# Kernel optimization log

Hardware: AMD Instinct MI355X
Metric: run time of the kernel (lower is better)

The kernel has to match this reference:

```python
import jax, jax.numpy as jnp
import numpy as np

D = 1024
H = 16
DH = D // H


def setup_inputs() -> dict:
    key = jax.random.key(0)
    ks = jax.random.split(key, 5)
    x = jax.random.normal(ks[0], (2, 2048, D), dtype=jnp.float32)
    s = 1.0 / np.sqrt(D)
    W_qkv = jax.random.normal(ks[1], (D, 3 * D), dtype=jnp.float32) * s
    b_qkv = jnp.zeros((3 * D,), dtype=jnp.float32)
    W_out = jax.random.normal(ks[2], (D, D), dtype=jnp.float32) * s
    b_out = jnp.zeros((D,), dtype=jnp.float32)
    return {"x": x, "W_qkv": W_qkv, "b_qkv": b_qkv, "W_out": W_out, "b_out": b_out}


def reference(x, W_qkv, b_qkv, W_out, b_out):
    B, N, _ = x.shape
    qkv = x @ W_qkv + b_qkv                       # [B,N,3D]
    qkv = qkv.reshape(B, N, 3, H, DH)
    q = jnp.transpose(qkv[:, :, 0], (0, 2, 1, 3))  # [B,H,N,DH]
    k = jnp.transpose(qkv[:, :, 1], (0, 2, 1, 3))
    v = jnp.transpose(qkv[:, :, 2], (0, 2, 1, 3))
    scores = jnp.einsum('bhnd,bhmd->bhnm', q, k) / jnp.sqrt(jnp.float32(DH))
    attn = jax.nn.softmax(scores, axis=-1)
    out = jnp.einsum('bhnm,bhmd->bhnd', attn, v)   # [B,H,N,DH]
    out = jnp.transpose(out, (0, 2, 1, 3)).reshape(B, N, D)
    return out @ W_out + b_out
```

## Files before the change

kernel.cpp:

```cpp
#include <hip/hip_runtime.h>

typedef unsigned short u16;
typedef unsigned int u32;
typedef __attribute__((ext_vector_type(8))) short bf16x8;
typedef __attribute__((ext_vector_type(4))) float f32x4;

static __device__ __forceinline__ void mfma16(f32x4& c, bf16x8 a, bf16x8 b) {
  asm("v_mfma_f32_16x16x32_bf16 %0, %1, %2, %0" : "+v"(c) : "v"(a), "v"(b));
}
static __device__ __forceinline__ float exp2_fast(float x) {
  float r; asm("v_exp_f32 %0, %1" : "=v"(r) : "v"(x)); return r;
}
static __device__ __forceinline__ u32 cvt_pk_bf16(float lo, float hi) {
  u32 r; asm("v_cvt_pk_bf16_f32 %0, %1, %2" : "=v"(r) : "v"(lo), "v"(hi)); return r;
}

static __device__ __forceinline__ float bfly_sum(float x) {
  x += __shfl_xor(x, 16);
  x += __shfl_xor(x, 32);
  return x;
}

static __device__ __forceinline__ u16 f2bf(float f) {
  union { float f; u32 u; } v; v.f = f;
  u32 r = v.u + 0x7fffu + ((v.u >> 16) & 1u);
  return (u16)(r >> 16);
}

typedef __attribute__((address_space(1))) void as1_v;
typedef __attribute__((address_space(3))) void as3_v;
static __device__ __forceinline__ void gload16(const u16* g, u16* l) {
  __builtin_amdgcn_global_load_lds((as1_v*)g, (as3_v*)l, 16, 0, 0);
}

__global__ __launch_bounds__(256) void cvt_bf16(const float* __restrict__ in,
                                                u16* __restrict__ out, int n4) {
  int i = blockIdx.x * 256 + threadIdx.x;
  if (i < n4) {
    float4 f = ((const float4*)in)[i];
    ushort4 u;
    u.x = f2bf(f.x); u.y = f2bf(f.y); u.z = f2bf(f.z); u.w = f2bf(f.w);
    ((ushort4*)out)[i] = u;
  }
}

__global__ __launch_bounds__(256) void transpose_cvt(const float* __restrict__ W,
                                                     u16* __restrict__ Wt,
                                                     int K, int Nc) {
  __shared__ float tile[32][33];
  int nb = blockIdx.x * 32, kb = blockIdx.y * 32;
  int tx = threadIdx.x, ty = threadIdx.y;
  for (int i = ty; i < 32; i += 8)
    tile[i][tx] = W[(size_t)(kb + i) * Nc + nb + tx];
  __syncthreads();
  for (int i = ty; i < 32; i += 8)
    Wt[(size_t)(nb + i) * K + kb + tx] = f2bf(tile[tx][i]);
}

__global__ __launch_bounds__(256) void vtrans(const u16* __restrict__ qkv,
                                              u16* __restrict__ vt) {
  __shared__ u16 t[64][72];
  const int tid = threadIdx.x;
  const int bh = blockIdx.y, nt = blockIdx.x;
  const int b = bh >> 4, h = bh & 15;
  const int n0 = nt * 64;
  const int r = tid >> 3, c = tid & 7;
  const u16* src = qkv + (size_t)(b * 2048 + n0 + r) * 3072 + 2048 + h * 64;
  *(int4*)&t[r][(c ^ ((r >> 3) & 7)) * 8] = *(const int4*)(src + c * 8);
  const u16* src2 = src + (size_t)32 * 3072;
  *(int4*)&t[r + 32][(c ^ (((r + 32) >> 3) & 7)) * 8] = *(const int4*)(src2 + c * 8);
  __syncthreads();
  const int d = tid >> 3, j0 = (tid & 7) * 8;
  union { int4 v; u16 u[8]; } o0, o1;
#pragma unroll
  for (int j = 0; j < 8; ++j) {
    const int row = j0 + j;
    const int sw = (row >> 3) & 7;
    o0.u[j] = t[row][((d >> 3) ^ sw) * 8 + (d & 7)];
    o1.u[j] = t[row][(((d + 32) >> 3) ^ sw) * 8 + ((d + 32) & 7)];
  }
  u16* dst = vt + (size_t)bh * 131072 + (size_t)d * 2048 + n0 + j0;
  *(int4*)dst = o0.v;
  *(int4*)(dst + (size_t)32 * 2048) = o1.v;
}

template <int OUT_F32>
__global__ __launch_bounds__(256) void gemm_bt(const u16* __restrict__ A,
                                               const u16* __restrict__ Bt,
                                               const float* __restrict__ bias,
                                               void* __restrict__ C,
                                               int M, int N, int K,
                                               float qscale, int qcols) {
  __shared__ u16 lA[2][4096];
  __shared__ u16 lB[2][4096];
  const int tid = threadIdx.x;
  const int lane = tid & 63, wid = tid >> 6;
  const int nbx = N >> 7;
  const int per = ((M >> 7) * nbx) >> 3;
  const int g = (blockIdx.x & 7) * per + (blockIdx.x >> 3);
  const int bx = g % nbx, by = g / nbx;
  const int m0 = by << 7, n0 = bx << 7;
  const int wr = wid >> 1, wc = wid & 1;

  const int srow = tid >> 2;
  const int scol = (tid & 3) << 3;
  const u16* gA0 = A + (size_t)(m0 + srow) * K + scol;
  const u16* gA1 = A + (size_t)(m0 + 64 + srow) * K + scol;
  const u16* gB0 = Bt + (size_t)(n0 + srow) * K + scol;
  const u16* gB1 = Bt + (size_t)(n0 + 64 + srow) * K + scol;

  const int rdA = (wr * 64 + (lane & 15)) * 32 + ((lane >> 4) * 8);
  const int rdB = (wc * 64 + (lane & 15)) * 32 + ((lane >> 4) * 8);

  f32x4 acc[4][4] = {};

  gload16(gA0, &lA[0][tid * 8]);
  gload16(gA1, &lA[0][2048 + tid * 8]);
  gload16(gB0, &lB[0][tid * 8]);
  gload16(gB1, &lB[0][2048 + tid * 8]);
  __syncthreads();

  const int nk = K >> 5;
  for (int t = 0; t < nk; ++t) {
    const int cur = t & 1, nxt = cur ^ 1;
    if (t + 1 < nk) {
      const int k0 = (t + 1) << 5;
      gload16(gA0 + k0, &lA[nxt][tid * 8]);
      gload16(gA1 + k0, &lA[nxt][2048 + tid * 8]);
      gload16(gB0 + k0, &lB[nxt][tid * 8]);
      gload16(gB1 + k0, &lB[nxt][2048 + tid * 8]);
    }
    bf16x8 aF[4], bF[4];
#pragma unroll
    for (int m = 0; m < 4; ++m) aF[m] = *(const bf16x8*)(&lA[cur][rdA + m * 512]);
#pragma unroll
    for (int n = 0; n < 4; ++n) bF[n] = *(const bf16x8*)(&lB[cur][rdB + n * 512]);
#pragma unroll
    for (int m = 0; m < 4; ++m)
#pragma unroll
      for (int n = 0; n < 4; ++n) mfma16(acc[m][n], aF[m], bF[n]);
    __syncthreads();
  }

#pragma unroll
  for (int n = 0; n < 4; ++n) {
    const int col = n0 + wc * 64 + n * 16 + (lane & 15);
    const float bv = bias[col];
    const float sc = (col < qcols) ? qscale : 1.0f;
#pragma unroll
    for (int m = 0; m < 4; ++m) {
      const int rbase = m0 + wr * 64 + m * 16 + ((lane >> 4) * 4);
#pragma unroll
      for (int r = 0; r < 4; ++r) {
        const float v = (acc[m][n][r] + bv) * sc;
        const size_t idx = (size_t)(rbase + r) * N + col;
        if (OUT_F32) ((float*)C)[idx] = v;
        else         ((u16*)C)[idx] = f2bf(v);
      }
    }
  }
}

__global__ __launch_bounds__(256) void gemm_bt_n64(const u16* __restrict__ A,
                                                   const u16* __restrict__ Bt,
                                                   const float* __restrict__ bias,
                                                   float* __restrict__ C,
                                                   int M, int N, int K) {
  __shared__ u16 lA[2][4096];
  __shared__ u16 lB[2][2048];
  const int tid = threadIdx.x;
  const int lane = tid & 63, wid = tid >> 6;
  const int nbx = N >> 6;
  const int per = ((M >> 7) * nbx) >> 3;
  const int g = (blockIdx.x & 7) * per + (blockIdx.x >> 3);
  const int bx = g % nbx, by = g / nbx;
  const int m0 = by << 7, n0 = bx << 6;
  const int wr = wid >> 1, wc = wid & 1;

  const int srow = tid >> 2;
  const int scol = (tid & 3) << 3;
  const u16* gA0 = A + (size_t)(m0 + srow) * K + scol;
  const u16* gA1 = A + (size_t)(m0 + 64 + srow) * K + scol;
  const u16* gB0 = Bt + (size_t)(n0 + srow) * K + scol;

  const int rdA = (wr * 64 + (lane & 15)) * 32 + ((lane >> 4) * 8);
  const int rdB = (wc * 32 + (lane & 15)) * 32 + ((lane >> 4) * 8);

  f32x4 acc[4][2] = {};

  gload16(gA0, &lA[0][tid * 8]);
  gload16(gA1, &lA[0][2048 + tid * 8]);
  gload16(gB0, &lB[0][tid * 8]);
  __syncthreads();

  const int nk = K >> 5;
  for (int t = 0; t < nk; ++t) {
    const int cur = t & 1, nxt = cur ^ 1;
    if (t + 1 < nk) {
      const int k0 = (t + 1) << 5;
      gload16(gA0 + k0, &lA[nxt][tid * 8]);
      gload16(gA1 + k0, &lA[nxt][2048 + tid * 8]);
      gload16(gB0 + k0, &lB[nxt][tid * 8]);
    }
    bf16x8 aF[4], bF[2];
#pragma unroll
    for (int m = 0; m < 4; ++m) aF[m] = *(const bf16x8*)(&lA[cur][rdA + m * 512]);
#pragma unroll
    for (int n = 0; n < 2; ++n) bF[n] = *(const bf16x8*)(&lB[cur][rdB + n * 512]);
#pragma unroll
    for (int m = 0; m < 4; ++m)
#pragma unroll
      for (int n = 0; n < 2; ++n) mfma16(acc[m][n], aF[m], bF[n]);
    __syncthreads();
  }

#pragma unroll
  for (int n = 0; n < 2; ++n) {
    const int col = n0 + wc * 32 + n * 16 + (lane & 15);
    const float bv = bias[col];
#pragma unroll
    for (int m = 0; m < 4; ++m) {
      const int rbase = m0 + wr * 64 + m * 16 + ((lane >> 4) * 4);
#pragma unroll
      for (int r = 0; r < 4; ++r)
        C[(size_t)(rbase + r) * N + col] = acc[m][n][r] + bv;
    }
  }
}

__global__ __launch_bounds__(256) void attn_kernel(const u16* __restrict__ qkv,
                                                   const u16* __restrict__ vt,
                                                   u16* __restrict__ attn_out) {
  __shared__ u16 lK[2][4096];
  __shared__ u16 lV[2][4096];

  const int tid = threadIdx.x, lane = tid & 63, w = tid >> 6;
  const int l15 = lane & 15, g = lane >> 4;
  const int bid = blockIdx.x;
  const int tt = bid >> 3;
  const int qt = tt & 31;
  const int bh = ((tt >> 5) << 3) | (bid & 7);
  const int b = bh >> 4, h = bh & 15;

  const size_t rowQ = (size_t)(b * 2048 + qt * 64 + w * 16 + l15);
  const u16* qptr = qkv + rowQ * 3072 + h * 64 + g * 8;
  const bf16x8 qf0 = *(const bf16x8*)(qptr);
  const bf16x8 qf1 = *(const bf16x8*)(qptr + 32);

  const int r0 = tid >> 3, r1 = 32 + (tid >> 3);
  const int c0 = (tid & 7) ^ ((r0 ^ (r0 >> 3)) & 7);
  const int c1 = (tid & 7) ^ ((r1 ^ (r1 >> 3)) & 7);
  const u16* gk0 = qkv + (size_t)(b * 2048 + r0) * 3072 + 1024 + h * 64 + c0 * 8;
  const u16* gk1 = qkv + (size_t)(b * 2048 + r1) * 3072 + 1024 + h * 64 + c1 * 8;
  const u16* vtb = vt + (size_t)bh * 131072;
  const u16* gv0 = vtb + (size_t)r0 * 2048 + c0 * 8;
  const u16* gv1 = vtb + (size_t)r1 * 2048 + c1 * 8;

  int koff[4][2];
#pragma unroll
  for (int f = 0; f < 4; ++f) {
    const int R = 32 * (f >> 1) + 8 * (l15 >> 2) + 4 * ((l15 >> 1) & 1) +
                  2 * (f & 1) + (l15 & 1);
    const int sw = (R ^ (R >> 3)) & 7;
#pragma unroll
    for (int hf = 0; hf < 2; ++hf)
      koff[f][hf] = R * 64 + ((((hf << 2) | g) ^ sw) << 3);
  }
  int voff[4][2];
#pragma unroll
  for (int d = 0; d < 4; ++d) {
    const int R = d * 16 + l15;
    const int sw = (R ^ (R >> 3)) & 7;
#pragma unroll
    for (int kk = 0; kk < 2; ++kk)
      voff[d][kk] = R * 64 + ((((kk << 2) | g) ^ sw) << 3);
  }

  float lp = 0.f;
  f32x4 oacc[4] = {};

  gload16(gk0, &lK[0][tid * 8]);
  gload16(gk1, &lK[0][2048 + tid * 8]);
  gload16(gv0, &lV[0][tid * 8]);
  gload16(gv1, &lV[0][2048 + tid * 8]);
  __syncthreads();

  for (int it = 0; it < 32; ++it) {
    const int cur = it & 1, nxt = cur ^ 1;
    const u16* Kc = lK[cur];
    const u16* Vc = lV[cur];
    if (it + 1 < 32) {
      const size_t ko = (size_t)(it + 1) * 64 * 3072;
      const int vo = (it + 1) * 64;
      gload16(gk0 + ko, &lK[nxt][tid * 8]);
      gload16(gk1 + ko, &lK[nxt][2048 + tid * 8]);
      gload16(gv0 + vo, &lV[nxt][tid * 8]);
      gload16(gv1 + vo, &lV[nxt][2048 + tid * 8]);
    }

    f32x4 s[4] = {};
#pragma unroll
    for (int f = 0; f < 4; ++f) {
      mfma16(s[f], *(const bf16x8*)(Kc + koff[f][0]), qf0);
      mfma16(s[f], *(const bf16x8*)(Kc + koff[f][1]), qf1);
    }

#pragma unroll
    for (int f = 0; f < 4; ++f)
#pragma unroll
      for (int r = 0; r < 4; ++r) s[f][r] = exp2_fast(s[f][r]);
    lp += (((s[0][0] + s[0][1]) + (s[0][2] + s[0][3])) +
           ((s[1][0] + s[1][1]) + (s[1][2] + s[1][3]))) +
          (((s[2][0] + s[2][1]) + (s[2][2] + s[2][3])) +
           ((s[3][0] + s[3][1]) + (s[3][2] + s[3][3])));

    union { bf16x8 v; u32 u[4]; } p0, p1;
    p0.u[0] = cvt_pk_bf16(s[0][0], s[0][1]);
    p0.u[1] = cvt_pk_bf16(s[1][0], s[1][1]);
    p0.u[2] = cvt_pk_bf16(s[0][2], s[0][3]);
    p0.u[3] = cvt_pk_bf16(s[1][2], s[1][3]);
    p1.u[0] = cvt_pk_bf16(s[2][0], s[2][1]);
    p1.u[1] = cvt_pk_bf16(s[3][0], s[3][1]);
    p1.u[2] = cvt_pk_bf16(s[2][2], s[2][3]);
    p1.u[3] = cvt_pk_bf16(s[3][2], s[3][3]);

#pragma unroll
    for (int d = 0; d < 4; ++d) {
      mfma16(oacc[d], *(const bf16x8*)(Vc + voff[d][0]), p0.v);
      mfma16(oacc[d], *(const bf16x8*)(Vc + voff[d][1]), p1.v);
    }

    __syncthreads();
  }

  const float l_ = bfly_sum(lp);
  const float inv = 1.f / l_;
#pragma unroll
  for (int d = 0; d < 4; ++d)
#pragma unroll
    for (int r = 0; r < 4; ++r)
      attn_out[rowQ * 1024 + h * 64 + d * 16 + g * 4 + r] = f2bf(oacc[d][r] * inv);
}

extern "C" void kernel_launch(void* const* d_in, const int* in_sizes, int n_in,
                              void* d_out, int out_size, void* d_ws, size_t ws_size,
                              hipStream_t stream) {
  const float* x    = (const float*)d_in[0];
  const float* Wqkv = (const float*)d_in[1];
  const float* bqkv = (const float*)d_in[2];
  const float* Wout = (const float*)d_in[3];
  const float* bout = (const float*)d_in[4];
  float* out = (float*)d_out;

  char* ws = (char*)d_ws;
  u16* xb    = (u16*)(ws);
  u16* vt    = (u16*)(ws);
  u16* WqkvT = (u16*)(ws + 8388608);
  u16* WoutT = (u16*)(ws + 14680064);
  u16* qkvb  = (u16*)(ws + 16777216);
  u16* attnb = (u16*)(ws + 41943040);

  cvt_bf16<<<4096, 256, 0, stream>>>(x, xb, 4194304 / 4);
  transpose_cvt<<<dim3(96, 32), dim3(32, 8), 0, stream>>>(Wqkv, WqkvT, 1024, 3072);
  transpose_cvt<<<dim3(32, 32), dim3(32, 8), 0, stream>>>(Wout, WoutT, 1024, 1024);

  gemm_bt<0><<<dim3(24 * 32), 256, 0, stream>>>(xb, WqkvT, bqkv, qkvb,
                                                4096, 3072, 1024, 0.18033688f, 1024);
  vtrans<<<dim3(32, 32), 256, 0, stream>>>(qkvb, vt);
  attn_kernel<<<dim3(32 * 32), 256, 0, stream>>>(qkvb, vt, attnb);
  gemm_bt_n64<<<dim3(512), 256, 0, stream>>>(attnb, WoutT, bout, out,
                                             4096, 1024, 1024);
}
```

Before: 129.0 us.

## Triple-buffer GEMM LDS tiles with prefetch distance two and partial vmcnt waits

Both bf16 GEMM kernels move from double to triple-buffered LDS staging, issuing global-to-LDS loads two K-steps ahead. The full __syncthreads is replaced by an explicit s_waitcnt vmcnt(N) plus barrier, so only the oldest tile's loads must land before the next iteration. This is meant to hide more global memory latency behind MFMA work. In exchange it uses 50% more LDS per block, which may lower occupancy, and it relies on hand-counted vmcnt values being correct.

```diff
diff --git a/kernel.cpp b/kernel.cpp
--- a/kernel.cpp
+++ b/kernel.cpp
@@ -32,6 +32,13 @@
 static __device__ __forceinline__ void gload16(const u16* g, u16* l) {
   __builtin_amdgcn_global_load_lds((as1_v*)g, (as3_v*)l, 16, 0, 0);
 }
+
+#define WAIT_BARRIER(N)                                   \
+  do {                                                    \
+    asm volatile("s_waitcnt vmcnt(" #N ")" ::: "memory"); \
+    __builtin_amdgcn_s_barrier();                         \
+    __builtin_amdgcn_sched_barrier(0);                    \
+  } while (0)
 
 __global__ __launch_bounds__(256) void cvt_bf16(const float* __restrict__ in,
                                                 u16* __restrict__ out, int n4) {
@@ -91,8 +98,8 @@
                                                void* __restrict__ C,
                                                int M, int N, int K,
                                                float qscale, int qcols) {
-  __shared__ u16 lA[2][4096];
-  __shared__ u16 lB[2][4096];
+  __shared__ u16 lA[3][4096];
+  __shared__ u16 lB[3][4096];
   const int tid = threadIdx.x;
   const int lane = tid & 63, wid = tid >> 6;
   const int nbx = N >> 7;
@@ -118,28 +125,36 @@
   gload16(gA1, &lA[0][2048 + tid * 8]);
   gload16(gB0, &lB[0][tid * 8]);
   gload16(gB1, &lB[0][2048 + tid * 8]);
-  __syncthreads();
+  gload16(gA0 + 32, &lA[1][tid * 8]);
+  gload16(gA1 + 32, &lA[1][2048 + tid * 8]);
+  gload16(gB0 + 32, &lB[1][tid * 8]);
+  gload16(gB1 + 32, &lB[1][2048 + tid * 8]);
+  WAIT_BARRIER(4);
 
   const int nk = K >> 5;
   for (int t = 0; t < nk; ++t) {
-    const int cur = t & 1, nxt = cur ^ 1;
+    const int cur = t % 3;
+    if (t + 2 < nk) {
+      const int kk = (t + 2) << 5;
+      const int nb = (t + 2) % 3;
+      gload16(gA0 + kk, &lA[nb][tid * 8]);
+      gload16(gA1 + kk, &lA[nb][2048 + tid * 8]);
+      gload16(gB0 + kk, &lB[nb][tid * 8]);
+      gload16(gB1 + kk, &lB[nb][2048 + tid * 8]);
+    }
+    bf16x8 aF[4], bF[4];
+#pragma unroll
+    for (int m = 0; m < 4; ++m) aF[m] = *(const bf16x8*)(&lA[cur][rdA + m * 512]);
+#pragma unroll
+    for (int n = 0; n < 4; ++n) bF[n] = *(const bf16x8*)(&lB[cur][rdB + n * 512]);
+#pragma unroll
+    for (int m = 0; m < 4; ++m)
+#pragma unroll
+      for (int n = 0; n < 4; ++n) mfma16(acc[m][n], aF[m], bF[n]);
     if (t + 1 < nk) {
-      const int k0 = (t + 1) << 5;
-      gload16(gA0 + k0, &lA[nxt][tid * 8]);
-      gload16(gA1 + k0, &lA[nxt][2048 + tid * 8]);
-      gload16(gB0 + k0, &lB[nxt][tid * 8]);
-      gload16(gB1 + k0, &lB[nxt][2048 + tid * 8]);
-    }
-    bf16x8 aF[4], bF[4];
-#pragma unroll
-    for (int m = 0; m < 4; ++m) aF[m] = *(const bf16x8*)(&lA[cur][rdA + m * 512]);
-#pragma unroll
-    for (int n = 0; n < 4; ++n) bF[n] = *(const bf16x8*)(&lB[cur][rdB + n * 512]);
-#pragma unroll
-    for (int m = 0; m < 4; ++m)
-#pragma unroll
-      for (int n = 0; n < 4; ++n) mfma16(acc[m][n], aF[m], bF[n]);
-    __syncthreads();
+      if (t + 2 < nk) WAIT_BARRIER(4);
+      else            WAIT_BARRIER(0);
+    }
   }
 
 #pragma unroll
@@ -166,8 +181,8 @@
                                                    const float* __restrict__ bias,
                                                    float* __restrict__ C,
                                                    int M, int N, int K) {
-  __shared__ u16 lA[2][4096];
-  __shared__ u16 lB[2][2048];
+  __shared__ u16 lA[3][4096];
+  __shared__ u16 lB[3][2048];
   const int tid = threadIdx.x;
   const int lane = tid & 63, wid = tid >> 6;
   const int nbx = N >> 6;
@@ -191,27 +206,34 @@
   gload16(gA0, &lA[0][tid * 8]);
   gload16(gA1, &lA[0][2048 + tid * 8]);
   gload16(gB0, &lB[0][tid * 8]);
-  __syncthreads();
+  gload16(gA0 + 32, &lA[1][tid * 8]);
+  gload16(gA1 + 32, &lA[1][2048 + tid * 8]);
+  gload16(gB0 + 32, &lB[1][tid * 8]);
+  WAIT_BARRIER(3);
 
   const int nk = K >> 5;
   for (int t = 0; t < nk; ++t) {
-    const int cur = t & 1, nxt = cur ^ 1;
+    const int cur = t % 3;
+    if (t + 2 < nk) {
+      const int kk = (t + 2) << 5;
+      const int nb = (t + 2) % 3;
+      gload16(gA0 + kk, &lA[nb][tid * 8]);
+      gload16(gA1 + kk, &lA[nb][2048 + tid * 8]);
+      gload16(gB0 + kk, &lB[nb][tid * 8]);
+    }
+    bf16x8 aF[4], bF[2];
+#pragma unroll
+    for (int m = 0; m < 4; ++m) aF[m] = *(const bf16x8*)(&lA[cur][rdA + m * 512]);
+#pragma unroll
+    for (int n = 0; n < 2; ++n) bF[n] = *(const bf16x8*)(&lB[cur][rdB + n * 512]);
+#pragma unroll
+    for (int m = 0; m < 4; ++m)
+#pragma unroll
+      for (int n = 0; n < 2; ++n) mfma16(acc[m][n], aF[m], bF[n]);
     if (t + 1 < nk) {
-      const int k0 = (t + 1) << 5;
-      gload16(gA0 + k0, &lA[nxt][tid * 8]);
-      gload16(gA1 + k0, &lA[nxt][2048 + tid * 8]);
-      gload16(gB0 + k0, &lB[nxt][tid * 8]);
-    }
-    bf16x8 aF[4], bF[2];
-#pragma unroll
-    for (int m = 0; m < 4; ++m) aF[m] = *(const bf16x8*)(&lA[cur][rdA + m * 512]);
-#pragma unroll
-    for (int n = 0; n < 2; ++n) bF[n] = *(const bf16x8*)(&lB[cur][rdB + n * 512]);
-#pragma unroll
-    for (int m = 0; m < 4; ++m)
-#pragma unroll
-      for (int n = 0; n < 2; ++n) mfma16(acc[m][n], aF[m], bF[n]);
-    __syncthreads();
+      if (t + 2 < nk) WAIT_BARRIER(3);
+      else            WAIT_BARRIER(0);
+    }
   }
 
 #pragma unroll
```

New measurement: 130.3 us. No clear change (+1.0%).
